# Performance work log

Hardware: AMD Instinct MI355X
Metric: run time of the kernel (lower is better)

Reference implementation:

```python
import jax, jax.numpy as jnp
import numpy as np

B, S, D = 2, 2048, 2048
H, KVH, HD = 16, 8, 128
EPS = 1e-6
ROPE_THETA = 10000.0


def _rope_cache(seq_len, head_dim):
    inv_freq = 1.0 / (ROPE_THETA ** (np.arange(0, head_dim, 2, dtype=np.float32) / head_dim))
    t = np.arange(seq_len, dtype=np.float32)
    freqs = np.outer(t, inv_freq)                      # [S, HD/2]
    emb = np.concatenate([freqs, freqs], axis=-1)      # [S, HD]
    return jnp.asarray(np.cos(emb)), jnp.asarray(np.sin(emb))


def setup_inputs() -> dict:
    key = jax.random.key(0)
    ks = jax.random.split(key, 10)
    x = jax.random.normal(ks[0], (B, S, D), dtype=jnp.float32)
    wq_q = jax.random.randint(ks[1], (H * HD, D), -127, 128, dtype=jnp.int32)
    wk_q = jax.random.randint(ks[2], (KVH * HD, D), -127, 128, dtype=jnp.int32)
    wv_q = jax.random.randint(ks[3], (KVH * HD, D), -127, 128, dtype=jnp.int32)
    wo_q = jax.random.randint(ks[4], (D, H * HD), -127, 128, dtype=jnp.int32)
    # per-output-channel scales (realistic small magnitudes)
    wq_s = jax.random.uniform(ks[5], (H * HD,), minval=1e-3, maxval=2e-2)
    wk_s = jax.random.uniform(ks[6], (KVH * HD,), minval=1e-3, maxval=2e-2)
    wv_s = jax.random.uniform(ks[7], (KVH * HD,), minval=1e-3, maxval=2e-2)
    wo_s = jax.random.uniform(ks[8], (D,), minval=1e-3, maxval=2e-2)
    q_norm_w = jnp.ones((HD,), dtype=jnp.float32)
    k_norm_w = jnp.ones((HD,), dtype=jnp.float32)
    cos_cache, sin_cache = _rope_cache(S, HD)
    return {"x": x, "wq_q": wq_q, "wq_s": wq_s, "wk_q": wk_q, "wk_s": wk_s,
            "wv_q": wv_q, "wv_s": wv_s, "wo_q": wo_q, "wo_s": wo_s,
            "q_norm_w": q_norm_w, "k_norm_w": k_norm_w,
            "cos_cache": cos_cache, "sin_cache": sin_cache}


def _dequant_linear(x, wq, ws):
    # W8A16-style: dequantize int8 weight with per-channel scale, then GEMM
    w = wq.astype(jnp.float32) * ws[:, None]   # [out, in]
    return x @ w.T


def _rms_norm(x, w, eps=EPS):
    var = jnp.mean(x * x, axis=-1, keepdims=True)
    return x * jax.lax.rsqrt(var + eps) * w


def _rotate_half(x):
    x1, x2 = jnp.split(x, 2, axis=-1)
    return jnp.concatenate([-x2, x1], axis=-1)


def _apply_rope(q, k, cos, sin):
    # q: [B,S,H,HD], k: [B,S,KVH,HD]; cos/sin: [S,HD] -> broadcast over batch, heads
    cos = cos[None, :, None, :]
    sin = sin[None, :, None, :]
    q = q * cos + _rotate_half(q) * sin
    k = k * cos + _rotate_half(k) * sin
    return q, k


def reference(x, wq_q, wq_s, wk_q, wk_s, wv_q, wv_s, wo_q, wo_s,
              q_norm_w, k_norm_w, cos_cache, sin_cache):
    batch, seq_len, dim = x.shape
    q = _dequant_linear(x, wq_q, wq_s).reshape(batch, seq_len, H, HD)
    k = _dequant_linear(x, wk_q, wk_s).reshape(batch, seq_len, KVH, HD)
    v = _dequant_linear(x, wv_q, wv_s).reshape(batch, seq_len, KVH, HD)
    q = _rms_norm(q, q_norm_w)
    k = _rms_norm(k, k_norm_w)
    # first forward: cache is empty -> kv = current k,v
    q, k = _apply_rope(q, k, cos_cache[:seq_len], sin_cache[:seq_len])
    q = q.transpose(0, 2, 1, 3)   # [B,H,S,HD]
    k = k.transpose(0, 2, 1, 3)   # [B,KVH,S,HD]
    v = v.transpose(0, 2, 1, 3)
    rep = H // KVH
    k = jnp.repeat(k, rep, axis=1)  # GQA repeat_interleave -> [B,H,S,HD]
    v = jnp.repeat(v, rep, axis=1)
    scale = 1.0 / jnp.sqrt(jnp.asarray(HD, dtype=x.dtype))
    scores = jnp.einsum('bhqd,bhkd->bhqk', q, k) * scale
    causal = jnp.tril(jnp.ones((seq_len, seq_len), dtype=bool))
    scores = jnp.where(causal[None, None], scores, jnp.finfo(scores.dtype).min)
    attn = jax.nn.softmax(scores, axis=-1)
    out = jnp.einsum('bhqk,bhkd->bhqd', attn, v)
    out = out.transpose(0, 2, 1, 3).reshape(batch, seq_len, H * HD)
    return _dequant_linear(out, wo_q, wo_s)
```

## Files before the change

### kernel.cpp

```cpp
#include <hip/hip_runtime.h>


typedef __attribute__((ext_vector_type(4))) float floatx4;
typedef __attribute__((ext_vector_type(8))) short short8v;
typedef __attribute__((ext_vector_type(4))) short short4v;
typedef __attribute__((ext_vector_type(8))) unsigned short ushort8v;

#define DEVINL __device__ __forceinline__

constexpr int cB = 2, cS = 2048, cD = 2048, cH = 16, cKVH = 8, cHD = 128;
constexpr int cM = cB * cS;
constexpr int cNqkv = (cH + 2 * cKVH) * cHD;
constexpr float cEPS = 1e-6f;
constexpr float cSCL2 = 0.08838834764831845f * 1.4426950408889634f;

DEVINL unsigned short f2bf(float f) {
  unsigned u = __float_as_uint(f);
  unsigned r = ((u >> 16) & 1u) + 0x7FFFu;
  return (unsigned short)((u + r) >> 16);
}
DEVINL float bf2f(unsigned short h) { return __uint_as_float(((unsigned)h) << 16); }

DEVINL floatx4 mfma_bf16(short8v a, short8v b, floatx4 c) {
  return __builtin_amdgcn_mfma_f32_16x16x32_bf16(a, b, c, 0, 0, 0);
}

DEVINL floatx4 mfma_pv(short4v a, short4v b, floatx4 c) {
#if __has_builtin(__builtin_amdgcn_mfma_f32_16x16x16bf16_1k)
  return __builtin_amdgcn_mfma_f32_16x16x16bf16_1k(a, b, c, 0, 0, 0);
#else
  short8v a8 = {a[0], a[1], a[2], a[3], (short)0, (short)0, (short)0, (short)0};
  short8v b8 = {b[0], b[1], b[2], b[3], (short)0, (short)0, (short)0, (short)0};
  return __builtin_amdgcn_mfma_f32_16x16x32_bf16(a8, b8, c, 0, 0, 0);
#endif
}

DEVINL void gl_lds16(const void* g, void* l) {
  __builtin_amdgcn_global_load_lds(
      (const __attribute__((address_space(1))) void*)g,
      (__attribute__((address_space(3))) void*)l, 16, 0, 0);
}

__global__ void detect_dtype(const unsigned* __restrict__ x, int* __restrict__ flag) {
  __shared__ int cnt;
  if (threadIdx.x == 0) cnt = 0;
  __syncthreads();
  int c = 0;
  for (int i = threadIdx.x; i < 4096; i += 256) {
    unsigned e = (x[i] >> 7) & 0xFFu;
    c += (e >= 100u && e <= 142u) ? 1 : 0;
  }
  atomicAdd(&cnt, c);
  __syncthreads();
  if (threadIdx.x == 0) *flag = (cnt > 2457) ? 1 : 0;
}

__global__ void conv_small(const void* p9, const void* p10, const void* p2,
                           const void* p4, const void* p6, const void* p8,
                           float* __restrict__ nw, float* __restrict__ scat,
                           float* __restrict__ so, const int* __restrict__ flag) {
  int i = blockIdx.x * 256 + threadIdx.x;
  int f = *flag;
  auto rd = [&](const void* p, int idx) -> float {
    return f ? bf2f(((const unsigned short*)p)[idx]) : ((const float*)p)[idx];
  };
  if (i < 256) {
    nw[i] = (i < 128) ? rd(p9, i) : rd(p10, i - 128);
  } else if (i < 256 + 4096) {
    int j = i - 256;
    scat[j] = (j < 2048) ? rd(p2, j) : (j < 3072 ? rd(p4, j - 2048) : rd(p6, j - 3072));
  } else if (i < 256 + 4096 + 2048) {
    int j = i - 4352;
    so[j] = rd(p8, j);
  }
}

__global__ void rope_pack(const void* __restrict__ cosc, const void* __restrict__ sinc,
                          float2* __restrict__ tab, const int* __restrict__ flag) {
  int i = blockIdx.x * 256 + threadIdx.x;
  if (i >= cS * 64) return;
  int s = i >> 6, t = i & 63;
  int f = *flag;
  float c = f ? bf2f(((const unsigned short*)cosc)[s * cHD + t])
              : ((const float*)cosc)[s * cHD + t];
  float sn = f ? bf2f(((const unsigned short*)sinc)[s * cHD + t])
               : ((const float*)sinc)[s * cHD + t];
  tab[i] = make_float2(c, sn);
}

DEVINL void pack_body(const void* src, unsigned short* dst, int K, int md,
                      int Trow, int Tdst, int kc, int tid, float L[16][264]) {
#pragma unroll
  for (int it = 0; it < 16; it++) {
    int e = it * 256 + tid;
    int r = e >> 8, c = e & 255;
    size_t idx = (size_t)(Trow * 16 + r) * K + kc * 256 + c;
    float v;
    if (md == 1)      v = ((const float*)src)[idx];
    else if (md == 2) v = (float)((const int*)src)[idx];
    else              v = bf2f(((const unsigned short*)src)[idx]);
    L[r][c] = v;
  }
  __syncthreads();
  const int lane = tid & 63, w = tid >> 6;
  const int q = lane >> 4, l16 = lane & 15;
#pragma unroll
  for (int p = 0; p < 2; p++) {
    int kbl = w + p * 4;
    ushort8v o;
#pragma unroll
    for (int j = 0; j < 8; j++) o[j] = f2bf(L[l16][kbl * 32 + q * 8 + j]);
    *(ushort8v*)(dst + ((size_t)Tdst * 64 + kc * 8 + kbl) * 512 + lane * 8) = o;
  }
}

__global__ __launch_bounds__(256) void pack_frag(
    const void* __restrict__ src, unsigned short* __restrict__ dst,
    int K, int mode, const int* __restrict__ flag) {
  __shared__ float L[16][264];
  int md = mode;
  if (md == 0) md = (*flag) ? 3 : 1;
  pack_body(src, dst, K, md, blockIdx.x, blockIdx.x, blockIdx.y, threadIdx.x, L);
}

__global__ __launch_bounds__(256) void pack_wqkv(
    const int* __restrict__ wq, const int* __restrict__ wk,
    const int* __restrict__ wv, unsigned short* __restrict__ dst) {
  __shared__ float L[16][264];
  int T = blockIdx.x;
  const int* src;
  int Trow;
  if (T < 128)      { src = wq; Trow = T; }
  else if (T < 192) { src = wk; Trow = T - 128; }
  else              { src = wv; Trow = T - 192; }
  pack_body(src, dst, 2048, 2, Trow, T, blockIdx.y, threadIdx.x, L);
}

DEVINL void gemm_core4(const unsigned short* __restrict__ Ap,
                       const unsigned short* __restrict__ Bp,
                       int tm0, int tn0, int nkb, int lane,
                       floatx4 acc[4][4]) {
  const unsigned short* ap[4];
  const unsigned short* bp[4];
#pragma unroll
  for (int i = 0; i < 4; i++) {
    ap[i] = Ap + ((size_t)(tm0 + i) * 64) * 512 + lane * 8;
    bp[i] = Bp + ((size_t)(tn0 + i) * 64) * 512 + lane * 8;
  }
  short8v a[4][4], b[4][4];
#pragma unroll
  for (int p = 0; p < 4; p++)
#pragma unroll
    for (int i = 0; i < 4; i++) {
      a[p][i] = *(const short8v*)(ap[i] + p * 512);
      b[p][i] = *(const short8v*)(bp[i] + p * 512);
    }
  for (int kb = 0; kb < nkb; kb += 4) {
    const bool more = (kb + 4) < nkb;
#pragma unroll
    for (int p = 0; p < 4; p++) {
#pragma unroll
      for (int mt = 0; mt < 4; mt++)
#pragma unroll
        for (int nt = 0; nt < 4; nt++)
          acc[mt][nt] = mfma_bf16(a[p][mt], b[p][nt], acc[mt][nt]);
      if (more) {
        const int o = (kb + 4 + p) * 512;
#pragma unroll
        for (int i = 0; i < 4; i++) {
          a[p][i] = *(const short8v*)(ap[i] + o);
          b[p][i] = *(const short8v*)(bp[i] + o);
        }
      }
    }
  }
}

__global__ __launch_bounds__(256) void gemm_qkv(
    const unsigned short* __restrict__ Ap, const unsigned short* __restrict__ Bp,
    const float* __restrict__ colscale, const float2* __restrict__ ropetab,
    const float* __restrict__ nw, unsigned short* __restrict__ Qb,
    unsigned short* __restrict__ Kb, unsigned short* __restrict__ Vt) {
  __shared__ float4 smem4[2192];
  char* smem = (char*)smem4;
  const int tid = threadIdx.x;
  const int lane = tid & 63, wave = tid >> 6;
  const int q = lane >> 4, l16 = lane & 15;
  const int m0 = blockIdx.y * 128, n0 = blockIdx.x * 128;
  const int wm = (wave & 1) * 64, wn = (wave >> 1) * 64;

  floatx4 acc[4][4] = {};
  gemm_core4(Ap, Bp, (m0 + wm) >> 4, (n0 + wn) >> 4, cD / 32, lane, acc);

  float sc[4];
#pragma unroll
  for (int nt = 0; nt < 4; nt++) sc[nt] = colscale[n0 + wn + nt * 16 + l16];
#pragma unroll
  for (int mt = 0; mt < 4; mt++)
#pragma unroll
    for (int nt = 0; nt < 4; nt++)
#pragma unroll
      for (int rg = 0; rg < 4; rg++) acc[mt][nt][rg] *= sc[nt];

  const int tile_n = blockIdx.x;
  const int bi = m0 >> 11, sbase = m0 & (cS - 1);

  if (tile_n >= 24) {
    unsigned short* T = (unsigned short*)smem;
#pragma unroll
    for (int mt = 0; mt < 4; mt++)
#pragma unroll
      for (int nt = 0; nt < 4; nt++) {
        short4v pk;
#pragma unroll
        for (int rg = 0; rg < 4; rg++) pk[rg] = (short)f2bf(acc[mt][nt][rg]);
        *(short4v*)(T + (wn + nt * 16 + l16) * 136 + (wm + mt * 16 + q * 4)) = pk;
      }
    __syncthreads();
    const int d = tid >> 1, sh = (tid & 1) * 64;
    unsigned short* dst = Vt + ((size_t)(bi * cKVH + (tile_n - 24)) * cHD + d) * cS
                          + sbase + sh;
#pragma unroll
    for (int j = 0; j < 8; j++)
      *(ushort8v*)(dst + j * 8) = *(const ushort8v*)(T + d * 136 + sh + j * 8);
  } else {
    unsigned short* W = (unsigned short*)smem;
    float* ssq  = (float*)(smem + 32768);
    float* invs = (float*)(smem + 33792);

    float sl[4][4];
#pragma unroll
    for (int mt = 0; mt < 4; mt++)
#pragma unroll
      for (int rg = 0; rg < 4; rg++) {
        float s = 0.f;
#pragma unroll
        for (int nt = 0; nt < 4; nt++) s += acc[mt][nt][rg] * acc[mt][nt][rg];
        s += __shfl_xor(s, 1); s += __shfl_xor(s, 2);
        s += __shfl_xor(s, 4); s += __shfl_xor(s, 8);
        sl[mt][rg] = s;
      }
    unsigned short* Wo = W + wave * 4096;
#pragma unroll
    for (int mt = 0; mt < 4; mt++)
#pragma unroll
      for (int nt = 0; nt < 4; nt++) {
        short4v pk;
#pragma unroll
        for (int rg = 0; rg < 4; rg++) pk[rg] = (short)f2bf(acc[mt][nt][rg]);
        *(short4v*)(Wo + (mt * 4 + nt) * 256 + lane * 4) = pk;
      }
    if (l16 == 0) {
#pragma unroll
      for (int mt = 0; mt < 4; mt++)
#pragma unroll
        for (int rg = 0; rg < 4; rg++)
          ssq[((wave >> 1) & 1) * 128 + wm + mt * 16 + q * 4 + rg] = sl[mt][rg];
    }
    __syncthreads();
    if (tid < 128)
      invs[tid] = rsqrtf((ssq[tid] + ssq[128 + tid]) * (1.0f / cHD) + cEPS);
    __syncthreads();

    const unsigned short* Wp = W + (wave ^ 2) * 4096;
    const int wn1 = wave >> 1;
    const float* nwb = nw + (tile_n < 16 ? 0 : cHD);
    float wown[4], wpar[4];
#pragma unroll
    for (int nt = 0; nt < 4; nt++) {
      wown[nt] = nwb[wn1 * 64 + nt * 16 + l16];
      wpar[nt] = nwb[(wn1 ^ 1) * 64 + nt * 16 + l16];
    }
    unsigned short* dstb = (tile_n < 16)
        ? Qb + ((size_t)(bi * cH + tile_n) * cS) * cHD
        : Kb + ((size_t)(bi * cKVH + (tile_n - 16)) * cS) * cHD;
#pragma unroll
    for (int mt = 0; mt < 4; mt++) {
      float iv[4];
#pragma unroll
      for (int rg = 0; rg < 4; rg++) iv[rg] = invs[wm + mt * 16 + q * 4 + rg];
#pragma unroll
      for (int nt = 0; nt < 4; nt++) {
        short4v pk = *(const short4v*)(Wp + (mt * 4 + nt) * 256 + lane * 4);
#pragma unroll
        for (int rg = 0; rg < 4; rg++) {
          int srow = sbase + wm + mt * 16 + q * 4 + rg;
          float2 cs = ropetab[srow * 64 + nt * 16 + l16];
          float nown = acc[mt][nt][rg] * iv[rg] * wown[nt];
          float npar = bf2f((unsigned short)pk[rg]) * iv[rg] * wpar[nt];
          float o = wn1 == 0 ? nown * cs.x - npar * cs.y
                             : nown * cs.x + npar * cs.y;
          dstb[(size_t)srow * cHD + wn1 * 64 + nt * 16 + l16] = f2bf(o);
        }
      }
    }
  }
}

__global__ __launch_bounds__(256) void gemm_out(
    const unsigned short* __restrict__ Ap, const unsigned short* __restrict__ Bp,
    const float* __restrict__ colscale, void* __restrict__ Cout,
    const int* __restrict__ flag, int N, int nkb) {
  const int tid = threadIdx.x;
  const int lane = tid & 63, wave = tid >> 6;
  const int q = lane >> 4, l16 = lane & 15;
  const int m0 = blockIdx.y * 128, n0 = blockIdx.x * 128;
  const int wm = (wave & 1) * 64, wn = (wave >> 1) * 64;

  floatx4 acc[4][4] = {};
  gemm_core4(Ap, Bp, (m0 + wm) >> 4, (n0 + wn) >> 4, nkb, lane, acc);

  const int f = *flag;
#pragma unroll
  for (int mt = 0; mt < 4; mt++) {
    int r0 = m0 + wm + mt * 16 + q * 4;
#pragma unroll
    for (int nt = 0; nt < 4; nt++) {
      int cn = n0 + wn + nt * 16 + l16;
      float sc = colscale[cn];
#pragma unroll
      for (int rg = 0; rg < 4; rg++) {
        float v = acc[mt][nt][rg] * sc;
        if (f) ((unsigned short*)Cout)[(size_t)(r0 + rg) * N + cn] = f2bf(v);
        else   ((float*)Cout)[(size_t)(r0 + rg) * N + cn] = v;
      }
    }
  }
}

__global__ __launch_bounds__(256, 2) void attn(
    const unsigned short* __restrict__ Qb, const unsigned short* __restrict__ Kb,
    const unsigned short* __restrict__ Vt, unsigned short* __restrict__ AOp) {
  __shared__ unsigned short SM[32768];
  const int tid = threadIdx.x;
  const int lane = tid & 63, wv = tid >> 6;
  const int q = lane >> 4, l16 = lane & 15;
  const int bi = blockIdx.z, h = blockIdx.y;
  const int kh = h >> 1;
  const int qt = (int)gridDim.x - 1 - (int)blockIdx.x;
  const int q0 = qt * 64;
  const int q0w = q0 + wv * 16;

  const unsigned short* Qbase = Qb + ((size_t)(bi * cH + h) * cS + q0w) * cHD;
  const unsigned short* Kbase = Kb + ((size_t)(bi * cKVH + kh) * cS) * cHD;
  const unsigned short* Vbase = Vt + ((size_t)(bi * cKVH + kh) * cHD) * cS;

  short8v qa[4];
#pragma unroll
  for (int c = 0; c < 4; c++)
    qa[c] = *(const short8v*)(Qbase + (size_t)l16 * cHD + c * 32 + q * 8);

  floatx4 oacc[8] = {};
  float lp = 0.f;

  int koff[4], voff[4];
#pragma unroll
  for (int i = 0; i < 4; i++) {
    int s = (wv * 4 + i) * 64 + lane;
    int r = s >> 4, u = (s & 15) ^ (r & 15);
    koff[i] = r * cHD + u * 8;
    int d = s >> 3, uv = (s & 7) ^ (d & 7);
    voff[i] = d * cS + uv * 8;
  }

  auto stage = [&](int win) {
    const int buf = (win & 1) * 16384;
    const int kv0 = win * 64;
    unsigned short* Kdst = SM + buf + (wv * 4) * 512;
    unsigned short* Vdst = SM + buf + 8192 + (wv * 4) * 512;
#pragma unroll
    for (int i = 0; i < 4; i++)
      gl_lds16(Kbase + (size_t)kv0 * cHD + koff[i], Kdst + i * 512);
#pragma unroll
    for (int i = 0; i < 4; i++)
      gl_lds16(Vbase + (size_t)kv0 + voff[i], Vdst + i * 512);
  };

  stage(0);
  for (int win = 0; win <= qt; win++) {
    __syncthreads();
    if (win < qt) stage(win + 1);
    const unsigned short* Ks = SM + (win & 1) * 16384;
    const unsigned short* Vs = Ks + 8192;

    floatx4 sres[4] = {};
#pragma unroll
    for (int c = 0; c < 4; c++) {
      short8v kf[4];
#pragma unroll
      for (int ntk = 0; ntk < 4; ntk++)
        kf[ntk] = *(const short8v*)(Ks + (ntk * 16 + l16) * 128 + (((c * 4 + q) ^ l16) * 8));
#pragma unroll
      for (int ntk = 0; ntk < 4; ntk++)
        sres[ntk] = mfma_bf16(kf[ntk], qa[c], sres[ntk]);
    }

    const bool lastwin = (win == qt);
    short4v pa[4];
#pragma unroll
    for (int ntk = 0; ntk < 4; ntk++) {
#pragma unroll
      for (int rg = 0; rg < 4; rg++) {
        float e = exp2f(sres[ntk][rg] * cSCL2);
        if (lastwin && (ntk * 16 + q * 4 + rg > wv * 16 + l16)) e = 0.f;
        lp += e;
        pa[ntk][rg] = (short)f2bf(e);
      }
    }

#pragma unroll
    for (int ntk = 0; ntk < 4; ntk++) {
#pragma unroll
      for (int db = 0; db < 8; db++) {
        short4v vb = *(const short4v*)(Vs + (db * 16 + l16) * 64 +
                       (((ntk * 2 + (q >> 1)) ^ (l16 & 7)) * 8 + (q & 1) * 4));
        oacc[db] = mfma_pv(pa[ntk], vb, oacc[db]);
      }
    }
  }

  float lf = lp;
  lf += __shfl_xor(lf, 16);
  lf += __shfl_xor(lf, 32);
  float li[4];
#pragma unroll
  for (int rg = 0; rg < 4; rg++) li[rg] = 1.0f / __shfl(lf, q * 4 + rg);

  __syncthreads();
  unsigned short* T = SM + wv * 16 * 136;
#pragma unroll
  for (int rg = 0; rg < 4; rg++)
#pragma unroll
    for (int db = 0; db < 8; db++)
      T[(q * 4 + rg) * 136 + db * 16 + l16] = f2bf(oacc[db][rg] * li[rg]);
  const int mtile = (bi * cS + q0w) >> 4;
#pragma unroll
  for (int kbl = 0; kbl < 4; kbl++) {
    short8v fr = *(const short8v*)(T + l16 * 136 + kbl * 32 + q * 8);
    *(short8v*)(AOp + ((size_t)mtile * 64 + h * 4 + kbl) * 512 + lane * 8) = fr;
  }
}

extern "C" void kernel_launch(void* const* d_in, const int* in_sizes, int n_in,
                              void* d_out, int out_size, void* d_ws, size_t ws_size,
                              hipStream_t stream) {
  (void)in_sizes; (void)n_in; (void)out_size; (void)ws_size;
  char* ws = (char*)d_ws;
  size_t off = 0;
  auto alloc = [&](size_t bytes) -> char* {
    char* p = ws + off;
    off += (bytes + 255) & ~((size_t)255);
    return p;
  };
  int* flag            = (int*)alloc(256);
  float2* ropetab      = (float2*)alloc((size_t)cS * 64 * 8);
  float* nw            = (float*)alloc(256 * 4);
  float* scat          = (float*)alloc(4096 * 4);
  float* so            = (float*)alloc(2048 * 4);
  unsigned short* xp   = (unsigned short*)alloc((size_t)cM * cD * 2);
  unsigned short* wp   = (unsigned short*)alloc((size_t)cNqkv * cD * 2);
  unsigned short* wop  = (unsigned short*)alloc((size_t)cD * cH * cHD * 2);
  unsigned short* Qb   = (unsigned short*)alloc((size_t)cB * cH * cS * cHD * 2);
  unsigned short* Kb   = (unsigned short*)alloc((size_t)cB * cKVH * cS * cHD * 2);
  unsigned short* Vt   = (unsigned short*)alloc((size_t)cB * cKVH * cHD * cS * 2);
  unsigned short* AOp  = (unsigned short*)alloc((size_t)cM * cD * 2);

  detect_dtype<<<1, 256, 0, stream>>>((const unsigned*)d_in[0], flag);
  conv_small<<<25, 256, 0, stream>>>(d_in[9], d_in[10], d_in[2], d_in[4], d_in[6],
                                     d_in[8], nw, scat, so, flag);
  rope_pack<<<(cS * 64 + 255) / 256, 256, 0, stream>>>(d_in[11], d_in[12], ropetab, flag);
  pack_frag<<<dim3(256, 8), 256, 0, stream>>>(d_in[0], xp, 2048, 0, flag);
  pack_wqkv<<<dim3(256, 8), 256, 0, stream>>>((const int*)d_in[1], (const int*)d_in[3],
                                              (const int*)d_in[5], wp);
  pack_frag<<<dim3(128, 8), 256, 0, stream>>>(d_in[7], wop, 2048, 2, flag);

  gemm_qkv<<<dim3(cNqkv / 128, cM / 128), 256, 0, stream>>>(
      xp, wp, scat, ropetab, nw, Qb, Kb, Vt);
  attn<<<dim3(cS / 64, cH, cB), 256, 0, stream>>>(Qb, Kb, Vt, AOp);
  gemm_out<<<dim3(cD / 128, cM / 128), 256, 0, stream>>>(
      AOp, wop, so, d_out, flag, cD, (cH * cHD) / 32);
}
```

Before: 423.5 us.

## Read V directly from global and use 32-deep PV MFMA with permuted K rows

The attention kernel stops staging V in LDS and instead loads V fragments straight from global memory per lane. It permutes K rows during staging so that the score layout matches the operand layout of the 16x16x32 MFMA, which lets PV use the wider instruction instead of 16x16x16. LDS use is halved and launch bounds are raised to 4 blocks per SM for more occupancy. Query tiles are also assigned with a rotated mapping across heads and batches to balance the causal workload. The risk is extra global/L2 traffic and latency from the uncached V loads.

```diff
diff --git a/kernel.cpp b/kernel.cpp
--- a/kernel.cpp
+++ b/kernel.cpp
@@ -23,16 +23,6 @@
 
 DEVINL floatx4 mfma_bf16(short8v a, short8v b, floatx4 c) {
   return __builtin_amdgcn_mfma_f32_16x16x32_bf16(a, b, c, 0, 0, 0);
-}
-
-DEVINL floatx4 mfma_pv(short4v a, short4v b, floatx4 c) {
-#if __has_builtin(__builtin_amdgcn_mfma_f32_16x16x16bf16_1k)
-  return __builtin_amdgcn_mfma_f32_16x16x16bf16_1k(a, b, c, 0, 0, 0);
-#else
-  short8v a8 = {a[0], a[1], a[2], a[3], (short)0, (short)0, (short)0, (short)0};
-  short8v b8 = {b[0], b[1], b[2], b[3], (short)0, (short)0, (short)0, (short)0};
-  return __builtin_amdgcn_mfma_f32_16x16x32_bf16(a8, b8, c, 0, 0, 0);
-#endif
 }
 
 DEVINL void gl_lds16(const void* g, void* l) {
@@ -328,16 +318,16 @@
   }
 }
 
-__global__ __launch_bounds__(256, 2) void attn(
+__global__ __launch_bounds__(256, 4) void attn(
     const unsigned short* __restrict__ Qb, const unsigned short* __restrict__ Kb,
     const unsigned short* __restrict__ Vt, unsigned short* __restrict__ AOp) {
-  __shared__ unsigned short SM[32768];
+  __shared__ unsigned short SM[16384];
   const int tid = threadIdx.x;
   const int lane = tid & 63, wv = tid >> 6;
   const int q = lane >> 4, l16 = lane & 15;
   const int bi = blockIdx.z, h = blockIdx.y;
   const int kh = h >> 1;
-  const int qt = (int)gridDim.x - 1 - (int)blockIdx.x;
+  const int qt = ((int)blockIdx.x + 2 * h + 8 * bi) & 31;
   const int q0 = qt * 64;
   const int q0w = q0 + wv * 16;
 
@@ -353,35 +343,32 @@
   floatx4 oacc[8] = {};
   float lp = 0.f;
 
-  int koff[4], voff[4];
+  int koff[4];
 #pragma unroll
   for (int i = 0; i < 4; i++) {
     int s = (wv * 4 + i) * 64 + lane;
     int r = s >> 4, u = (s & 15) ^ (r & 15);
-    koff[i] = r * cHD + u * 8;
-    int d = s >> 3, uv = (s & 7) ^ (d & 7);
-    voff[i] = d * cS + uv * 8;
+    int sig = (r & 32) + ((r >> 2) & 3) * 8 + ((r >> 4) & 1) * 4 + (r & 3);
+    koff[i] = sig * cHD + u * 8;
   }
 
   auto stage = [&](int win) {
-    const int buf = (win & 1) * 16384;
+    const int buf = (win & 1) * 8192;
     const int kv0 = win * 64;
     unsigned short* Kdst = SM + buf + (wv * 4) * 512;
-    unsigned short* Vdst = SM + buf + 8192 + (wv * 4) * 512;
 #pragma unroll
     for (int i = 0; i < 4; i++)
       gl_lds16(Kbase + (size_t)kv0 * cHD + koff[i], Kdst + i * 512);
-#pragma unroll
-    for (int i = 0; i < 4; i++)
-      gl_lds16(Vbase + (size_t)kv0 + voff[i], Vdst + i * 512);
   };
+
+  const unsigned short* Vlane = Vbase + (size_t)l16 * cS + q * 8;
 
   stage(0);
   for (int win = 0; win <= qt; win++) {
     __syncthreads();
     if (win < qt) stage(win + 1);
-    const unsigned short* Ks = SM + (win & 1) * 16384;
-    const unsigned short* Vs = Ks + 8192;
+    const unsigned short* Ks = SM + (win & 1) * 8192;
+    const int kv0 = win * 64;
 
     floatx4 sres[4] = {};
 #pragma unroll
@@ -396,25 +383,27 @@
     }
 
     const bool lastwin = (win == qt);
-    short4v pa[4];
+    short8v pa8[2];
 #pragma unroll
     for (int ntk = 0; ntk < 4; ntk++) {
 #pragma unroll
       for (int rg = 0; rg < 4; rg++) {
         float e = exp2f(sres[ntk][rg] * cSCL2);
-        if (lastwin && (ntk * 16 + q * 4 + rg > wv * 16 + l16)) e = 0.f;
+        if (lastwin) {
+          int kvloc = (ntk >> 1) * 32 + q * 8 + (ntk & 1) * 4 + rg;
+          if (kvloc > wv * 16 + l16) e = 0.f;
+        }
         lp += e;
-        pa[ntk][rg] = (short)f2bf(e);
-      }
-    }
-
-#pragma unroll
-    for (int ntk = 0; ntk < 4; ntk++) {
+        pa8[ntk >> 1][(ntk & 1) * 4 + rg] = (short)f2bf(e);
+      }
+    }
+
+#pragma unroll
+    for (int t = 0; t < 2; t++) {
 #pragma unroll
       for (int db = 0; db < 8; db++) {
-        short4v vb = *(const short4v*)(Vs + (db * 16 + l16) * 64 +
-                       (((ntk * 2 + (q >> 1)) ^ (l16 & 7)) * 8 + (q & 1) * 4));
-        oacc[db] = mfma_pv(pa[ntk], vb, oacc[db]);
+        short8v vb = *(const short8v*)(Vlane + (size_t)(db * 16) * cS + kv0 + t * 32);
+        oacc[db] = mfma_bf16(pa8[t], vb, oacc[db]);
       }
     }
   }
```

New measurement: 490.0 us. 15.7% more time.
